# Kernel tuning notes

Measured on AMD Instinct MI355X. Metric: run time of the kernel, lower is better.

## Reference

```python
import jax, jax.numpy as jnp
import numpy as np

N, D = 8192, 256
E = 65536


def setup_inputs() -> dict:
    key = jax.random.key(0)
    ks = jax.random.split(key, 16)
    s = 1.0 / np.sqrt(D)  # nn.Linear default init scale
    return {
        "x_mean": jax.random.normal(ks[0], (N, D), dtype=jnp.float32),
        "x_var": jax.random.uniform(ks[1], (N, D), dtype=jnp.float32),
        "edge_index": jax.random.randint(ks[2], (2, E), 0, N, dtype=jnp.int64),
        "edge_timestamps": jax.random.uniform(ks[3], (E,), dtype=jnp.float32),
        "Wq": jax.random.uniform(ks[4], (D, D), jnp.float32, -s, s),
        "bq": jax.random.uniform(ks[5], (D,), jnp.float32, -s, s),
        "Wk": jax.random.uniform(ks[6], (D, D), jnp.float32, -s, s),
        "bk": jax.random.uniform(ks[7], (D,), jnp.float32, -s, s),
        "Wv": jax.random.uniform(ks[8], (D, D), jnp.float32, -s, s),
        "bv": jax.random.uniform(ks[9], (D,), jnp.float32, -s, s),
        "Wo": jax.random.uniform(ks[10], (D, D), jnp.float32, -s, s),
        "bo": jax.random.uniform(ks[11], (D,), jnp.float32, -s, s),
        "Wvar": jax.random.uniform(ks[12], (D, D), jnp.float32, -s, s),
        "bvar": jax.random.uniform(ks[13], (D,), jnp.float32, -s, s),
    }


def reference(x_mean, x_var, edge_index, edge_timestamps,
              Wq, bq, Wk, bk, Wv, bv, Wo, bo, Wvar, bvar):
    # edge_index / edge_timestamps are accepted but unused (as in the original forward).
    head_dim = D // 4  # num_heads=4; heads are never split, only used for scale
    scale = head_dim ** -0.5

    q = x_mean @ Wq.T + bq  # [N, D]
    k = x_mean @ Wk.T + bk
    v = x_mean @ Wv.T + bv

    attn = jax.nn.softmax((q @ k.T) * scale, axis=-1)  # [N, N] (dropout: eval mode)

    out_mean = (attn @ v) @ Wo.T + bo  # [N, D]

    v_var = x_var @ Wvar.T + bvar
    out_var = (attn * attn) @ v_var  # squared weights against projected variance
    return out_mean, out_var
```

## Files before the change

### kernel.cpp

```cpp
#include <hip/hip_runtime.h>
#include <hip/hip_bf16.h>
#include <hip/hip_fp16.h>

#define DEV __device__ __forceinline__

typedef __attribute__((ext_vector_type(8))) _Float16 h8;
typedef __attribute__((ext_vector_type(4))) float floatx4;

DEV float bf2f(unsigned short b) { return __uint_as_float(((unsigned)b) << 16); }

DEV void async_ld16(const void* g, void* l) {
  __builtin_amdgcn_global_load_lds(
      (const __attribute__((address_space(1))) unsigned int*)g,
      (__attribute__((address_space(3))) unsigned int*)l, 16, 0, 0);
}

DEV int detect_bf16(const void* x_mean) {
  const unsigned* w = (const unsigned*)x_mean;
  unsigned v = w[threadIdx.x & 63];
  unsigned ex = (v >> 7) & 0xFFu;
  int vote = (ex >= 100u && ex <= 144u) ? 1 : 0;
  unsigned long long b = __ballot(vote);
  return __popcll(b) >= 48 ? 1 : 0;
}

DEV float load_elem(const void* p, int isbf, size_t i) {
  return isbf ? bf2f(((const unsigned short*)p)[i]) : ((const float*)p)[i];
}

DEV void stage8h(const void* src, int isbf, size_t idx, float scale, _Float16* dst) {
  h8 o;
  if (isbf) {
    const unsigned short* s = (const unsigned short*)src + idx;
#pragma unroll
    for (int j = 0; j < 8; ++j) o[j] = (_Float16)(bf2f(s[j]) * scale);
  } else {
    const float* f = (const float*)src + idx;
    float4 a = *(const float4*)f;
    float4 b = *(const float4*)(f + 4);
    o[0] = (_Float16)(a.x * scale); o[1] = (_Float16)(a.y * scale);
    o[2] = (_Float16)(a.z * scale); o[3] = (_Float16)(a.w * scale);
    o[4] = (_Float16)(b.x * scale); o[5] = (_Float16)(b.y * scale);
    o[6] = (_Float16)(b.z * scale); o[7] = (_Float16)(b.w * scale);
  }
  *(h8*)dst = o;
}

struct ProjArgs {
  const void* A[4];
  const void* B[4];
  const void* bias[4];
  _Float16* C[4];
  int fl_tpc[4];
  float scale[4];
  int bias_row[4];
  const void* xdet;
};

__global__ __launch_bounds__(256) void proj_kernel(ProjArgs p) {
  __shared__ __align__(16) char smem[34816];
  _Float16* As = (_Float16*)smem;
  _Float16* Bs = As + 4096;
  _Float16* Ts = (_Float16*)smem;
  int isbf = detect_bf16(p.xdet);
  int z = blockIdx.z;
  size_t i0, j0;
  if (z < 2) { i0 = (size_t)blockIdx.x * 128; j0 = (size_t)blockIdx.y * 128; }
  else       { i0 = (size_t)blockIdx.y * 128; j0 = (size_t)blockIdx.x * 128; }
  const void* A = p.A[z];
  const void* B = p.B[z];
  const void* bias = p.bias[z];
  const float scale = p.scale[z];
  const int bias_row = p.bias_row[z];
  const int tpc = p.fl_tpc[z];
  _Float16* C = p.C[z];
  const int t = threadIdx.x;
  const int lane = t & 63, wave = t >> 6;
  const int wr = wave >> 1, wc = wave & 1;
  const int q = lane >> 4, m = lane & 15;
  floatx4 acc[4][4] = {};
  for (int k0 = 0; k0 < 256; k0 += 32) {
#pragma unroll
    for (int it = 0; it < 2; ++it) {
      int e = it * 2048 + t * 8;
      int row = e >> 5, col = e & 31;
      stage8h(A, isbf, (i0 + row) * (size_t)256 + k0 + col, 1.f, &As[e]);
      stage8h(B, isbf, (j0 + row) * (size_t)256 + k0 + col, 1.f, &Bs[e]);
    }
    __syncthreads();
    h8 af[4], bfr[4];
#pragma unroll
    for (int r = 0; r < 4; ++r)
      af[r] = *(const h8*)&As[(wr * 64 + r * 16 + m) * 32 + q * 8];
#pragma unroll
    for (int c = 0; c < 4; ++c)
      bfr[c] = *(const h8*)&Bs[(wc * 64 + c * 16 + m) * 32 + q * 8];
#pragma unroll
    for (int r = 0; r < 4; ++r)
#pragma unroll
      for (int c = 0; c < 4; ++c)
        acc[r][c] = __builtin_amdgcn_mfma_f32_16x16x32_f16(af[r], bfr[c], acc[r][c], 0, 0, 0);
    __syncthreads();
  }
#pragma unroll
  for (int r = 0; r < 4; ++r)
#pragma unroll
    for (int c = 0; c < 4; ++c) {
      size_t col = j0 + wc * 64 + c * 16 + m;
      float bcol = bias_row ? 0.f : load_elem(bias, isbf, col);
#pragma unroll
      for (int g = 0; g < 4; ++g) {
        size_t row = i0 + wr * 64 + r * 16 + q * 4 + g;
        float val = acc[r][c][g] + bcol;
        if (bias_row) val += load_elem(bias, isbf, row);
        Ts[(wr * 64 + r * 16 + q * 4 + g) * 136 + wc * 64 + c * 16 + m] =
            (_Float16)(val * scale);
      }
    }
  __syncthreads();
  size_t ti0 = i0 >> 4, tj0 = j0 >> 5;
#pragma unroll
  for (int it = 0; it < 8; ++it) {
    int cch = it * 4 + wave;
    int ci = cch >> 2, ck = cch & 3;
    int il = ci * 16 + (lane & 15);
    int jl = ck * 32 + (lane >> 4) * 8;
    h8 v = *(const h8*)&Ts[il * 136 + jl];
    *(h8*)&C[((ti0 + ci) * (size_t)tpc + (tj0 + ck)) * 512 + lane * 8] = v;
  }
}

__global__ __launch_bounds__(256) void zero_rs_kernel(float* __restrict__ rs) {
  rs[blockIdx.x * 256 + threadIdx.x] = 0.f;
}

__global__ __launch_bounds__(512, 4) void flash_kernel(
    const _Float16* __restrict__ qb, const _Float16* __restrict__ kb,
    const _Float16* __restrict__ vT, const _Float16* __restrict__ vvT,
    float* __restrict__ rs, float* __restrict__ otm4, float* __restrict__ otv4) {
  __shared__ __align__(16) _Float16 Qs[32 * 512];
  __shared__ __align__(16) _Float16 Ks[32 * 512];
  __shared__ __align__(16) _Float16 Ps[16 * 512];
  const size_t NP = 2097152;
  const int t = threadIdx.x;
  const int lane = t & 63, wave = t >> 6;
  const int hi = lane >> 4, m = lane & 15;
  const int wid = blockIdx.x;
  const int xcd = wid & 7;
  const int z = xcd >> 1;
  const size_t bx = (size_t)((xcd & 1) * 64 + (wid >> 3));
  const int wq = wave >> 2, wk = wave & 3;
  const int wq2 = wave >> 2, wd = wave & 3;

#pragma unroll
  for (int it = 0; it < 4; ++it) {
    int tile = it * 8 + wave;
    async_ld16(&qb[((bx * 4 + (size_t)(tile >> 3)) * 8 + (tile & 7)) * 512 + lane * 8],
               &Qs[tile * 512 + lane * 8]);
  }
  floatx4 accm[2][4] = {}, accv[2][4] = {};
  float rsum[2][4] = {};
  const size_t kvRowBase = (size_t)z * 128;
  for (int kvt = 0; kvt < 16; ++kvt) {
    floatx4 s[2][2] = {};
    const size_t kvRow0 = kvRowBase + kvt * 8;
#pragma unroll
    for (int ko = 0; ko < 2; ++ko) {
#pragma unroll
      for (int it = 0; it < 4; ++it)
        async_ld16(&kb[((kvRow0 + wave) * 8 + (size_t)(ko * 4 + it)) * 512 + lane * 8],
                   &Ks[(wave * 4 + it) * 512 + lane * 8]);
      __syncthreads();
#pragma unroll
      for (int kt2 = 0; kt2 < 4; ++kt2) {
        h8 af[2], bf[2];
#pragma unroll
        for (int r = 0; r < 2; ++r)
          af[r] = *(const h8*)&Qs[((wq * 2 + r) * 8 + ko * 4 + kt2) * 512 + lane * 8];
#pragma unroll
        for (int c = 0; c < 2; ++c)
          bf[c] = *(const h8*)&Ks[((wk * 2 + c) * 4 + kt2) * 512 + lane * 8];
#pragma unroll
        for (int r = 0; r < 2; ++r)
#pragma unroll
          for (int c = 0; c < 2; ++c)
            s[r][c] = __builtin_amdgcn_mfma_f32_16x16x32_f16(af[r], bf[c], s[r][c], 0, 0, 0);
      }
      __syncthreads();
    }
#pragma unroll
    for (int r = 0; r < 2; ++r)
#pragma unroll
      for (int c = 0; c < 2; ++c) {
        int lp = hi * 4 + 16 * (2 * c + (m >> 3));
        _Float16* dst = &Ps[((wq * 2 + r) * 4 + wk) * 512 + lp * 8 + (m & 7)];
#pragma unroll
        for (int g = 0; g < 4; ++g) {
          float e = __expf(fminf(s[r][c][g], 8.f)) * 0.015625f;
          rsum[r][g] += e;
          dst[g * 8] = (_Float16)e;
        }
      }
    __syncthreads();
    const size_t kvT0 = (size_t)z * 64 + kvt * 4;
#pragma unroll
    for (int ks = 0; ks < 4; ++ks) {
      h8 a[2], b1[4];
#pragma unroll
      for (int c = 0; c < 4; ++c)
        b1[c] = *(const h8*)&vT[((size_t)(wd * 4 + c) * 256 + kvT0 + ks) * 512 + lane * 8];
#pragma unroll
      for (int r = 0; r < 2; ++r)
        a[r] = *(const h8*)&Ps[((wq2 * 2 + r) * 4 + ks) * 512 + lane * 8];
#pragma unroll
      for (int r = 0; r < 2; ++r)
#pragma unroll
        for (int c = 0; c < 4; ++c)
          accm[r][c] = __builtin_amdgcn_mfma_f32_16x16x32_f16(a[r], b1[c], accm[r][c], 0, 0, 0);
    }
#pragma unroll
    for (int ks = 0; ks < 4; ++ks) {
      h8 a2[2], b2[4];
#pragma unroll
      for (int c = 0; c < 4; ++c)
        b2[c] = *(const h8*)&vvT[((size_t)(wd * 4 + c) * 256 + kvT0 + ks) * 512 + lane * 8];
#pragma unroll
      for (int r = 0; r < 2; ++r) {
        h8 a = *(const h8*)&Ps[((wq2 * 2 + r) * 4 + ks) * 512 + lane * 8];
        a2[r] = a * a;
      }
#pragma unroll
      for (int r = 0; r < 2; ++r)
#pragma unroll
        for (int c = 0; c < 4; ++c)
          accv[r][c] = __builtin_amdgcn_mfma_f32_16x16x32_f16(a2[r], b2[c], accv[r][c], 0, 0, 0);
    }
  }
#pragma unroll
  for (int r = 0; r < 2; ++r)
#pragma unroll
    for (int g = 0; g < 4; ++g) {
      float part = rsum[r][g];
      part += __shfl_xor(part, 1);
      part += __shfl_xor(part, 2);
      part += __shfl_xor(part, 4);
      part += __shfl_xor(part, 8);
      if (m == 0)
        unsafeAtomicAdd(&rs[bx * 64 + wq * 32 + r * 16 + hi * 4 + g], part);
    }
  float* om = otm4 + (size_t)z * NP;
  float* ov = otv4 + (size_t)z * NP;
#pragma unroll
  for (int r = 0; r < 2; ++r)
#pragma unroll
    for (int g = 0; g < 4; ++g) {
      size_t row = bx * 64 + wq2 * 32 + r * 16 + hi * 4 + g;
#pragma unroll
      for (int c = 0; c < 4; ++c) {
        size_t col = wd * 64 + c * 16 + m;
        om[row * 256 + col] = accm[r][c][g];
        ov[row * 256 + col] = accv[r][c][g];
      }
    }
}

__global__ __launch_bounds__(256) void final_kernel(const float* __restrict__ ot4,
                                                    const void* Wo, const void* bo,
                                                    const void* xdet,
                                                    const float* __restrict__ rs,
                                                    const float* __restrict__ otv4,
                                                    float* __restrict__ Cm,
                                                    float* __restrict__ Cv) {
  __shared__ __align__(16) _Float16 As[64 * 32];
  __shared__ __align__(16) _Float16 Bs[128 * 32];
  const size_t NP = 2097152;
  int isbf = detect_bf16(xdet);
  const int t = threadIdx.x;
  const int lane = t & 63, wave = t >> 6;
  const int wr = wave >> 1, wc = wave & 1;
  const int q = lane >> 4, m = lane & 15;
  const size_t i0 = (size_t)blockIdx.x * 64, j0 = (size_t)blockIdx.y * 128;
  floatx4 acc[2][4] = {};
  for (int k0 = 0; k0 < 256; k0 += 32) {
    {
      int e = t * 8;
      int row = e >> 5, col = e & 31;
      size_t idx = (i0 + row) * (size_t)256 + k0 + col;
      h8 o;
#pragma unroll
      for (int h = 0; h < 2; ++h) {
        float4 a0 = *(const float4*)&ot4[idx + h * 4];
        float4 a1 = *(const float4*)&ot4[NP + idx + h * 4];
        float4 a2 = *(const float4*)&ot4[2 * NP + idx + h * 4];
        float4 a3 = *(const float4*)&ot4[3 * NP + idx + h * 4];
        o[h * 4 + 0] = (_Float16)(a0.x + a1.x + a2.x + a3.x);
        o[h * 4 + 1] = (_Float16)(a0.y + a1.y + a2.y + a3.y);
        o[h * 4 + 2] = (_Float16)(a0.z + a1.z + a2.z + a3.z);
        o[h * 4 + 3] = (_Float16)(a0.w + a1.w + a2.w + a3.w);
      }
      *(h8*)&As[t * 8] = o;
    }
#pragma unroll
    for (int it = 0; it < 2; ++it) {
      int e = it * 2048 + t * 8;
      int row = e >> 5, col = e & 31;
      stage8h(Wo, isbf, (j0 + row) * (size_t)256 + k0 + col, 1.f, &Bs[e]);
    }
    __syncthreads();
    h8 af[2], bfr[4];
#pragma unroll
    for (int r = 0; r < 2; ++r)
      af[r] = *(const h8*)&As[(wr * 32 + r * 16 + m) * 32 + q * 8];
#pragma unroll
    for (int c = 0; c < 4; ++c)
      bfr[c] = *(const h8*)&Bs[(wc * 64 + c * 16 + m) * 32 + q * 8];
#pragma unroll
    for (int r = 0; r < 2; ++r)
#pragma unroll
      for (int c = 0; c < 4; ++c)
        acc[r][c] = __builtin_amdgcn_mfma_f32_16x16x32_f16(af[r], bfr[c], acc[r][c], 0, 0, 0);
    __syncthreads();
  }
#pragma unroll
  for (int r = 0; r < 2; ++r)
#pragma unroll
    for (int g = 0; g < 4; ++g) {
      size_t row = i0 + wr * 32 + r * 16 + q * 4 + g;
      float inv = 1.f / rs[row];
#pragma unroll
      for (int c = 0; c < 4; ++c) {
        size_t col = j0 + wc * 64 + c * 16 + m;
        float bcol = load_elem(bo, isbf, col);
        Cm[row * 256 + col] = acc[r][c][g] * inv + bcol;
      }
    }
#pragma unroll
  for (int it = 0; it < 8; ++it) {
    int e = it * 256 + t;
    int row = e >> 5, cg = e & 31;
    size_t rrow = i0 + row;
    float inv = 1.f / rs[rrow];
    float inv2 = inv * inv;
    size_t o = rrow * 256 + j0 + cg * 4;
    float4 v0 = *(const float4*)&otv4[o];
    float4 v1 = *(const float4*)&otv4[NP + o];
    float4 v2 = *(const float4*)&otv4[2 * NP + o];
    float4 v3 = *(const float4*)&otv4[3 * NP + o];
    float4 v;
    v.x = (v0.x + v1.x + v2.x + v3.x) * inv2;
    v.y = (v0.y + v1.y + v2.y + v3.y) * inv2;
    v.z = (v0.z + v1.z + v2.z + v3.z) * inv2;
    v.w = (v0.w + v1.w + v2.w + v3.w) * inv2;
    *(float4*)&Cv[o] = v;
  }
}

extern "C" void kernel_launch(void* const* d_in, const int* in_sizes, int n_in,
                              void* d_out, int out_size, void* d_ws, size_t ws_size,
                              hipStream_t stream) {
  const void* x_mean = d_in[0];
  const void* x_var  = d_in[1];
  const void* Wq   = d_in[4];
  const void* bq   = d_in[5];
  const void* Wk   = d_in[6];
  const void* bk   = d_in[7];
  const void* Wv   = d_in[8];
  const void* bv   = d_in[9];
  const void* Wo   = d_in[10];
  const void* bo   = d_in[11];
  const void* Wvar = d_in[12];
  const void* bvar = d_in[13];
  float* out = (float*)d_out;

  const size_t NE_S = 67108864;
  const size_t NE_P = 2097152;
  if (ws_size < (NE_S + 5 * NE_P) * 2) return;
  _Float16* w   = (_Float16*)d_ws;
  _Float16* qb  = w;
  _Float16* kb  = qb + NE_P;
  _Float16* vT  = kb + NE_P;
  _Float16* vvT = vT + NE_P;
  float* rs     = (float*)(vvT + NE_P);
  float* otm4   = rs + 8192;
  float* otv4   = otm4 + 4 * NE_P;

  ProjArgs p;
  p.A[0] = x_mean; p.B[0] = Wq;     p.bias[0] = bq;   p.C[0] = qb;  p.fl_tpc[0] = 8;   p.scale[0] = 0.125f; p.bias_row[0] = 0;
  p.A[1] = x_mean; p.B[1] = Wk;     p.bias[1] = bk;   p.C[1] = kb;  p.fl_tpc[1] = 8;   p.scale[1] = 1.f;    p.bias_row[1] = 0;
  p.A[2] = Wv;     p.B[2] = x_mean; p.bias[2] = bv;   p.C[2] = vT;  p.fl_tpc[2] = 256; p.scale[2] = 1.f;    p.bias_row[2] = 1;
  p.A[3] = Wvar;   p.B[3] = x_var;  p.bias[3] = bvar; p.C[3] = vvT; p.fl_tpc[3] = 256; p.scale[3] = 1.f;    p.bias_row[3] = 1;
  p.xdet = x_mean;

  zero_rs_kernel<<<dim3(32), 256, 0, stream>>>(rs);
  proj_kernel<<<dim3(64, 2, 4), 256, 0, stream>>>(p);
  flash_kernel<<<dim3(512), 512, 0, stream>>>(qb, kb, vT, vvT, rs, otm4, otv4);
  final_kernel<<<dim3(128, 2), 256, 0, stream>>>(otm4, Wo, bo, x_mean, rs, otv4, out, out + NE_P);
}
```

Before: 324.4 us.

## Repartition PV waves across columns and stage outputs through LDS for coalesced stores

```diff
diff --git a/kernel.cpp b/kernel.cpp
--- a/kernel.cpp
+++ b/kernel.cpp
@@ -138,9 +138,11 @@
     const _Float16* __restrict__ qb, const _Float16* __restrict__ kb,
     const _Float16* __restrict__ vT, const _Float16* __restrict__ vvT,
     float* __restrict__ rs, float* __restrict__ otm4, float* __restrict__ otv4) {
-  __shared__ __align__(16) _Float16 Qs[32 * 512];
-  __shared__ __align__(16) _Float16 Ks[32 * 512];
-  __shared__ __align__(16) _Float16 Ps[16 * 512];
+  __shared__ __align__(16) char smem[81920];
+  _Float16* Qs = (_Float16*)smem;
+  _Float16* Ks = (_Float16*)(smem + 32768);
+  _Float16* Ps = (_Float16*)(smem + 65536);
+  float* T = (float*)smem;
   const size_t NP = 2097152;
   const int t = threadIdx.x;
   const int lane = t & 63, wave = t >> 6;
@@ -150,7 +152,6 @@
   const int z = xcd >> 1;
   const size_t bx = (size_t)((xcd & 1) * 64 + (wid >> 3));
   const int wq = wave >> 2, wk = wave & 3;
-  const int wq2 = wave >> 2, wd = wave & 3;
 
 #pragma unroll
   for (int it = 0; it < 4; ++it) {
@@ -158,7 +159,7 @@
     async_ld16(&qb[((bx * 4 + (size_t)(tile >> 3)) * 8 + (tile & 7)) * 512 + lane * 8],
                &Qs[tile * 512 + lane * 8]);
   }
-  floatx4 accm[2][4] = {}, accv[2][4] = {};
+  floatx4 accm[4][2] = {}, accv[4][2] = {};
   float rsum[2][4] = {};
   const size_t kvRowBase = (size_t)z * 128;
   for (int kvt = 0; kvt < 16; ++kvt) {
@@ -205,34 +206,34 @@
     const size_t kvT0 = (size_t)z * 64 + kvt * 4;
 #pragma unroll
     for (int ks = 0; ks < 4; ++ks) {
-      h8 a[2], b1[4];
-#pragma unroll
-      for (int c = 0; c < 4; ++c)
-        b1[c] = *(const h8*)&vT[((size_t)(wd * 4 + c) * 256 + kvT0 + ks) * 512 + lane * 8];
-#pragma unroll
-      for (int r = 0; r < 2; ++r)
-        a[r] = *(const h8*)&Ps[((wq2 * 2 + r) * 4 + ks) * 512 + lane * 8];
-#pragma unroll
-      for (int r = 0; r < 2; ++r)
-#pragma unroll
-        for (int c = 0; c < 4; ++c)
+      h8 a[4], b1[2];
+#pragma unroll
+      for (int c = 0; c < 2; ++c)
+        b1[c] = *(const h8*)&vT[((size_t)(wave * 2 + c) * 256 + kvT0 + ks) * 512 + lane * 8];
+#pragma unroll
+      for (int r = 0; r < 4; ++r)
+        a[r] = *(const h8*)&Ps[(r * 4 + ks) * 512 + lane * 8];
+#pragma unroll
+      for (int r = 0; r < 4; ++r)
+#pragma unroll
+        for (int c = 0; c < 2; ++c)
           accm[r][c] = __builtin_amdgcn_mfma_f32_16x16x32_f16(a[r], b1[c], accm[r][c], 0, 0, 0);
     }
 #pragma unroll
     for (int ks = 0; ks < 4; ++ks) {
-      h8 a2[2], b2[4];
-#pragma unroll
-      for (int c = 0; c < 4; ++c)
-        b2[c] = *(const h8*)&vvT[((size_t)(wd * 4 + c) * 256 + kvT0 + ks) * 512 + lane * 8];
-#pragma unroll
-      for (int r = 0; r < 2; ++r) {
-        h8 a = *(const h8*)&Ps[((wq2 * 2 + r) * 4 + ks) * 512 + lane * 8];
+      h8 a2[4], b2[2];
+#pragma unroll
+      for (int c = 0; c < 2; ++c)
+        b2[c] = *(const h8*)&vvT[((size_t)(wave * 2 + c) * 256 + kvT0 + ks) * 512 + lane * 8];
+#pragma unroll
+      for (int r = 0; r < 4; ++r) {
+        h8 a = *(const h8*)&Ps[(r * 4 + ks) * 512 + lane * 8];
         a2[r] = a * a;
       }
 #pragma unroll
-      for (int r = 0; r < 2; ++r)
-#pragma unroll
-        for (int c = 0; c < 4; ++c)
+      for (int r = 0; r < 4; ++r)
+#pragma unroll
+        for (int c = 0; c < 2; ++c)
           accv[r][c] = __builtin_amdgcn_mfma_f32_16x16x32_f16(a2[r], b2[c], accv[r][c], 0, 0, 0);
     }
   }
@@ -248,20 +249,35 @@
       if (m == 0)
         unsafeAtomicAdd(&rs[bx * 64 + wq * 32 + r * 16 + hi * 4 + g], part);
     }
-  float* om = otm4 + (size_t)z * NP;
-  float* ov = otv4 + (size_t)z * NP;
-#pragma unroll
-  for (int r = 0; r < 2; ++r)
-#pragma unroll
-    for (int g = 0; g < 4; ++g) {
-      size_t row = bx * 64 + wq2 * 32 + r * 16 + hi * 4 + g;
-#pragma unroll
-      for (int c = 0; c < 4; ++c) {
-        size_t col = wd * 64 + c * 16 + m;
-        om[row * 256 + col] = accm[r][c][g];
-        ov[row * 256 + col] = accv[r][c][g];
-      }
-    }
+  float* om = otm4 + (size_t)z * NP + bx * (64 * 256);
+  float* ov = otv4 + (size_t)z * NP + bx * (64 * 256);
+#pragma unroll
+  for (int r = 0; r < 4; ++r)
+#pragma unroll
+    for (int c = 0; c < 2; ++c)
+#pragma unroll
+      for (int g = 0; g < 4; ++g)
+        T[(r * 16 + hi * 4 + g) * 256 + wave * 32 + c * 16 + m] = accm[r][c][g];
+  __syncthreads();
+#pragma unroll
+  for (int p = 0; p < 8; ++p) {
+    int f = p * 512 + t;
+    *(float4*)&om[f * 4] = *(const float4*)&T[f * 4];
+  }
+  __syncthreads();
+#pragma unroll
+  for (int r = 0; r < 4; ++r)
+#pragma unroll
+    for (int c = 0; c < 2; ++c)
+#pragma unroll
+      for (int g = 0; g < 4; ++g)
+        T[(r * 16 + hi * 4 + g) * 256 + wave * 32 + c * 16 + m] = accv[r][c][g];
+  __syncthreads();
+#pragma unroll
+  for (int p = 0; p < 8; ++p) {
+    int f = p * 512 + t;
+    *(float4*)&ov[f * 4] = *(const float4*)&T[f * 4];
+  }
 }
 
 __global__ __launch_bounds__(256) void final_kernel(const float* __restrict__ ot4,
```

After: 355.7 us. 1.1x slower.
